# Performance work log

Hardware: AMD Instinct MI355X
Metric: run time of the kernel (lower is better)

The kernel has to match this reference:

```python
import jax, jax.numpy as jnp
import numpy as np
from math import factorial

# ---- static config mirroring Cace.__init__ ----
MAX_L = 3            # max angular degree
N_RBF = 8            # Bessel radial basis size
RB = 8               # n_radial_basis (radial embedding dim after transform)
K = 3                # n_atom_basis -> edge channels C = K*K
NZ = 4               # len(zs)
CUTOFF = 5.5
N_NODES = 2000
N_EDGES = 50000
T_MP = 1             # num_message_passing
MP_NORM = 1.0 / np.sqrt(25.0)   # 1/sqrt(avg_num_neighbors)
C = K * K

def _lxlylz(max_l):
    out = []
    for l in range(max_l + 1):
        for lx in range(l, -1, -1):
            for ly in range(l - lx, -1, -1):
                out.append((lx, ly, l - lx - ly))
    return out

L_LIST = _lxlylz(MAX_L)                 # 20 Cartesian monomials for max_l=3
NL = len(L_LIST)
LX = np.array([t[0] for t in L_LIST]); LY = np.array([t[1] for t in L_LIST]); LZ = np.array([t[2] for t in L_LIST])
DEGS = LX + LY + LZ                     # degree l of each monomial
MULTI = np.array([factorial(int(d)) / (factorial(int(a)) * factorial(int(b)) * factorial(int(c)))
                  for a, b, c, d in zip(LX, LY, LZ, DEGS)], dtype=np.float32)
SEL = np.zeros((NL, MAX_L + 1), np.float32)
SEL[np.arange(NL), DEGS] = 1.0          # monomial -> degree one-hot (for per-l sums)
NB = 1 + (MAX_L + 1)                    # symmetrizer feats: nu=1 (l=0) + nu=2 per l

def bessel(r):  # [E] -> [E, N_RBF]
    n = jnp.arange(1, N_RBF + 1, dtype=r.dtype)
    return jnp.sqrt(2.0 / CUTOFF) * jnp.sin(n[None, :] * jnp.pi * r[:, None] / CUTOFF) / r[:, None]

def poly_cutoff(r):  # MACE-style polynomial cutoff, p=6
    p = 6.0
    u = r / CUTOFF
    f = 1.0 - (p + 1.0) * (p + 2.0) / 2.0 * u**6 + p * (p + 2.0) * u**7 - p * (p + 1.0) / 2.0 * u**8
    return f * (u < 1.0)

def axis_pows(x):  # [E] -> [E, MAX_L+1] = x^0..x^MAX_L (safe grads, handles negatives)
    pows = [jnp.ones_like(x)]
    for _ in range(MAX_L):
        pows.append(pows[-1] * x)
    return jnp.stack(pows, axis=1)

def angular(u):  # unit vectors [E,3] -> Cartesian monomials [E, NL]
    return axis_pows(u[:, 0])[:, LX] * axis_pows(u[:, 1])[:, LY] * axis_pows(u[:, 2])[:, LZ]

def radial_transform(x, W):  # x [N,R,L,C], W [MAX_L+1,R,Rb] shared per degree l
    return jnp.einsum('nrlc,lrb->nblc', x, W[DEGS])

def symmetrize(A):  # A [N,Rb,NL,C] -> B [N,Rb,NB,C]
    b1 = A[:, :, :1, :]  # nu=1: the (0,0,0) monomial (index 0)
    w = (A * A) * jnp.asarray(MULTI)[None, None, :, None]
    b2 = jnp.einsum('nrlc,lm->nrmc', w, jnp.asarray(SEL))  # nu=2 invariant per degree l
    return jnp.concatenate([b1, b2], axis=2)


def setup_inputs() -> dict:
    key = jax.random.key(0)
    ks = jax.random.split(key, 9)
    positions = jax.random.uniform(ks[0], (N_NODES, 3), dtype=jnp.float32) * 12.0
    species = jax.random.randint(ks[1], (N_NODES,), 0, NZ)
    send = jax.random.randint(ks[2], (N_EDGES,), 0, N_NODES)
    off = jax.random.randint(ks[3], (N_EDGES,), 1, N_NODES)
    recv = (send + off) % N_NODES  # no self-edges -> strictly positive edge lengths
    edge_index = jnp.stack([send, recv])
    shifts = jnp.zeros((N_EDGES, 3), jnp.float32)
    W_embed = jax.random.normal(ks[4], (NZ, K), jnp.float32)
    W_radial = jax.random.normal(ks[5], (MAX_L + 1, N_RBF, RB), jnp.float32) / np.sqrt(N_RBF)
    W_mem = jax.random.normal(ks[6], (MAX_L + 1, RB, RB), jnp.float32) / np.sqrt(RB)
    W_ar = jax.random.normal(ks[7], (N_RBF, RB), jnp.float32) / np.sqrt(N_RBF)
    W_chi = jax.random.normal(ks[8], (RB, NB), jnp.float32) * 0.1
    return {"positions": positions, "shifts": shifts, "W_embed": W_embed, "W_radial": W_radial,
            "W_mem": W_mem, "W_ar": W_ar, "W_chi": W_chi, "species": species, "edge_index": edge_index}


def reference(positions, shifts, W_embed, W_radial, W_mem, W_ar, W_chi, species, edge_index):
    n_nodes = positions.shape[0]
    send, recv = edge_index[0], edge_index[1]
    # edge geometry
    vec = positions[recv] - positions[send] + shifts
    lengths = jnp.linalg.norm(vec, axis=-1)
    u = vec / (lengths[:, None] + 1e-9)
    rad = bessel(lengths)          # [E,R]
    fcut = poly_cutoff(lengths)    # [E]
    ang = angular(u)               # [E,NL]
    # edge type encoding: outer product of sender/receiver species embeddings
    emb = W_embed[species]         # [N,K]
    enc = (emb[send][:, :, None] * emb[recv][:, None, :]).reshape(-1, C)  # [E,C]
    # elementwise_multiply_3tensors -> [E,R,NL,C]
    edge_attri = jnp.einsum('er,el,ec->erlc', rad * fcut[:, None], ang, enc)
    A = radial_transform(jax.ops.segment_sum(edge_attri, recv, num_segments=n_nodes), W_radial)  # [N,Rb,NL,C]
    B = symmetrize(A)              # [N,Rb,NB,C]
    feats = [B]
    for _ in range(T_MP):
        mem = jnp.einsum('nrlc,lrb->nblc', A, W_mem[DEGS])        # NodeMemory
        chi = jnp.einsum('nbkc,bk->nc', B, W_chi)                  # MessageBchi node scalar
        msg_bchi = edge_attri * chi[send][:, None, None, :]
        A_bchi = radial_transform(jax.ops.segment_sum(msg_bchi, recv, num_segments=n_nodes), W_radial)
        fr = (rad @ W_ar) * fcut[:, None]                          # MessageAr radial filter [E,Rb]
        msg_ar = A[send] * fr[:, :, None, None]
        A_ar = jax.ops.segment_sum(msg_ar, recv, num_segments=n_nodes)
        A = (A_ar + A_bchi) * MP_NORM + mem
        B = symmetrize(A)
        feats.append(B)
    return jnp.stack(feats, axis=-1)   # [N,Rb,NB,C,T_MP+1]
```

## Files before the change

### kernel.cpp

```cpp
#include <hip/hip_runtime.h>
#include <hip/hip_bf16.h>


#define CUTF 5.5f
#define MPNORM 0.2f
#define TILE 48
#define BG 8

__constant__ int   d_DEGS[20]  = {0,1,1,1,2,2,2,2,2,2,3,3,3,3,3,3,3,3,3,3};
__constant__ float d_MULTI[20] = {1,1,1,1,1,2,2,1,2,1,1,3,3,3,6,3,1,3,3,1};

__global__ void k_count(const int* __restrict__ eidx, int* __restrict__ counts, int E) {
  int e = blockIdx.x * blockDim.x + threadIdx.x;
  if (e < E) atomicAdd(&counts[eidx[E + e]], 1);
}

__global__ void k_scan(const int* __restrict__ counts, int* __restrict__ offs, int N) {
  __shared__ int part[256];
  int t = threadIdx.x;
  int local[8]; int sum = 0;
  #pragma unroll
  for (int i = 0; i < 8; i++) {
    int idx = t*8 + i;
    int v = (idx < N) ? counts[idx] : 0;
    local[i] = sum; sum += v;
  }
  part[t] = sum; __syncthreads();
  for (int d = 1; d < 256; d <<= 1) {
    int add = (t >= d) ? part[t-d] : 0;
    __syncthreads();
    part[t] += add;
    __syncthreads();
  }
  int excl = part[t] - sum;
  #pragma unroll
  for (int i = 0; i < 8; i++) {
    int idx = t*8 + i;
    if (idx < N) offs[idx] = excl + local[i];
  }
  if (t == 255) offs[N] = part[255];
}

__global__ void k_edge(const float* __restrict__ pos,
                       const float* __restrict__ shifts,
                       const float* __restrict__ Wemb,
                       const float* __restrict__ Wrad,
                       const float* __restrict__ War,
                       const int* __restrict__ species,
                       const int* __restrict__ eidx,
                       const int* __restrict__ offs,
                       int* __restrict__ cursor,
                       float* __restrict__ edata,
                       int* __restrict__ esend,
                       int E) {
  __shared__ float war_s[64];
  __shared__ float wrad_s[256];
  int t = threadIdx.x;
  if (t < 64) war_s[t] = War[t];
  wrad_s[t] = Wrad[t];
  __syncthreads();
  int e = blockIdx.x * blockDim.x + t;
  if (e >= E) return;
  int s  = eidx[e];
  int rI = eidx[E + e];
  float vx = pos[rI*3+0] - pos[s*3+0] + shifts[e*3+0];
  float vy = pos[rI*3+1] - pos[s*3+1] + shifts[e*3+1];
  float vz = pos[rI*3+2] - pos[s*3+2] + shifts[e*3+2];
  float len = sqrtf(vx*vx + vy*vy + vz*vz);
  float inv = 1.0f / (len + 1e-9f);
  float ux = vx*inv, uy = vy*inv, uz = vz*inv;
  float uu = len * (1.0f/CUTF);
  float u2 = uu*uu, u6 = u2*u2*u2;
  float fcut = (uu < 1.0f) ? (1.0f - 28.0f*u6 + 48.0f*u6*uu - 21.0f*u6*u2) : 0.0f;
  float x = 3.14159265358979f * uu;
  float sn = sinf(x), c2 = 2.0f*cosf(x), snm1 = 0.0f;
  float pref = sqrtf(2.0f/CUTF) / (len + 1e-20f);
  float rad[8], g[8];
  #pragma unroll
  for (int k = 0; k < 8; k++) {
    rad[k] = pref * sn;
    g[k]   = rad[k] * fcut;
    float nxt = c2*sn - snm1; snm1 = sn; sn = nxt;
  }
  float v[80];
  #pragma unroll
  for (int d = 0; d < 4; d++)
    #pragma unroll
    for (int b = 0; b < 8; b++) {
      float a = 0.0f;
      #pragma unroll
      for (int r = 0; r < 8; r++) a += g[r] * wrad_s[d*64 + r*8 + b];
      v[d*8+b] = a;
    }
  #pragma unroll
  for (int b = 0; b < 8; b++) {
    float a = 0.0f;
    #pragma unroll
    for (int k = 0; k < 8; k++) a += rad[k] * war_s[k*8+b];
    v[32+b] = a * fcut;
  }
  float px2 = ux*ux, py2 = uy*uy, pz2 = uz*uz;
  v[40] = 1.0f; v[41] = ux;     v[42] = uy;     v[43] = uz;
  v[44] = px2;  v[45] = ux*uy;  v[46] = ux*uz;  v[47] = py2;
  v[48] = uy*uz;v[49] = pz2;
  v[50] = px2*ux; v[51] = px2*uy; v[52] = px2*uz; v[53] = ux*py2;
  v[54] = ux*uy*uz; v[55] = ux*pz2; v[56] = py2*uy; v[57] = py2*uz;
  v[58] = uy*pz2; v[59] = pz2*uz;
  int zs = species[s], zr = species[rI];
  float es0 = Wemb[zs*3+0], es1 = Wemb[zs*3+1], es2 = Wemb[zs*3+2];
  float er0 = Wemb[zr*3+0], er1 = Wemb[zr*3+1], er2 = Wemb[zr*3+2];
  v[60] = es0*er0; v[61] = es0*er1; v[62] = es0*er2;
  v[63] = es1*er0; v[64] = es1*er1; v[65] = es1*er2;
  v[66] = es2*er0; v[67] = es2*er1; v[68] = es2*er2;
  #pragma unroll
  for (int w = 69; w < 80; w++) v[w] = 0.0f;
  int slot = atomicAdd(&cursor[rI], 1);
  int dst = offs[rI] + slot;
  float4* eb4 = reinterpret_cast<float4*>(edata + (size_t)dst * 80);
  #pragma unroll
  for (int w = 0; w < 20; w++)
    eb4[w] = make_float4(v[4*w], v[4*w+1], v[4*w+2], v[4*w+3]);
  esend[dst] = s;
}

__global__ __launch_bounds__(192) void k_nodeA(
    const float* __restrict__ edata, const int* __restrict__ offs,
    const float* __restrict__ Wchi,
    float* __restrict__ A, uint4* __restrict__ Abf4,
    float* __restrict__ chi, float* __restrict__ B0, int N) {
  __shared__ float wchi_s[40];
  __shared__ float Bsh[360];
  __shared__ __align__(16) float est[TILE*80];
  int t = threadIdx.x, n = blockIdx.x;
  for (int i = t; i < 40;  i += 192) wchi_s[i] = Wchi[i];
  for (int i = t; i < 360; i += 192) Bsh[i] = 0.0f;
  int l = t / 9, c = t - l*9;
  bool act = t < 180;
  int ll = act ? l : 0, cc = act ? c : 0;
  int deg = act ? d_DEGS[ll] : 0;
  float Ab[8];
  #pragma unroll
  for (int b = 0; b < 8; b++) Ab[b] = 0.0f;
  int start = offs[n], end = offs[n+1];
  for (int tb = start; tb < end; tb += TILE) {
    int cnt = min(TILE, end - tb);
    __syncthreads();
    const float4* src = reinterpret_cast<const float4*>(edata + (size_t)tb*80);
    float4* dst = reinterpret_cast<float4*>(est);
    for (int i = t; i < cnt*20; i += 192) dst[i] = src[i];
    __syncthreads();
    #pragma unroll 4
    for (int j = 0; j < cnt; j++) {
      const float* eb = est + j*80;
      float p = eb[40+ll] * eb[60+cc];
      const float4* gw4 = reinterpret_cast<const float4*>(eb + deg*8);
      float4 g0 = gw4[0], g1 = gw4[1];
      Ab[0] += p*g0.x; Ab[1] += p*g0.y; Ab[2] += p*g0.z; Ab[3] += p*g0.w;
      Ab[4] += p*g1.x; Ab[5] += p*g1.y; Ab[6] += p*g1.z; Ab[7] += p*g1.w;
    }
  }
  __syncthreads();
  if (act) {
    #pragma unroll
    for (int b = 0; b < 8; b++) A[(size_t)n*1440 + t*8 + b] = Ab[b];
    unsigned int pr[4];
    #pragma unroll
    for (int bp = 0; bp < 4; bp++) {
      __hip_bfloat16 blo = __float2bfloat16(Ab[2*bp]);
      __hip_bfloat16 bhi = __float2bfloat16(Ab[2*bp+1]);
      pr[bp] = (unsigned int)(*reinterpret_cast<unsigned short*>(&blo))
             | ((unsigned int)(*reinterpret_cast<unsigned short*>(&bhi)) << 16);
    }
    uint4 pk; pk.x = pr[0]; pk.y = pr[1]; pk.z = pr[2]; pk.w = pr[3];
    Abf4[(size_t)n*180 + t] = pk;
    if (l == 0) {
      #pragma unroll
      for (int b = 0; b < 8; b++) Bsh[b*45 + c] = Ab[b];
    }
    float mlt = d_MULTI[ll]; int kk = 1 + deg;
    #pragma unroll
    for (int b = 0; b < 8; b++) atomicAdd(&Bsh[b*45 + kk*9 + c], mlt*Ab[b]*Ab[b]);
  }
  __syncthreads();
  if (t < 9) {
    float s = 0.0f;
    for (int b = 0; b < 8; b++)
      #pragma unroll
      for (int kq = 0; kq < 5; kq++) s += Bsh[b*45 + kq*9 + t] * wchi_s[b*5 + kq];
    chi[n*9 + t] = s;
  }
  for (int i = t; i < 360; i += 192)
    B0[(size_t)n*360 + i] = Bsh[i];
}

__global__ __launch_bounds__(192) void k_node2(
    const float* __restrict__ edata, const int* __restrict__ esend,
    const int* __restrict__ offs, const float* __restrict__ Wmem,
    const float* __restrict__ A, const uint4* __restrict__ Abf4,
    const float* __restrict__ chi, const float* __restrict__ B0,
    float* __restrict__ out, int N) {
  __shared__ float wm_s[288];
  __shared__ float Bsh[360];
  __shared__ int   snd_s[BG];
  __shared__ float chi_s[BG*9];
  __shared__ __align__(16) float est[BG*80];
  __shared__ uint4 stg[BG*180];
  int t = threadIdx.x, n = blockIdx.x;
  for (int i = t; i < 256; i += 192) { int d = i >> 6, rm = i & 63; wm_s[d*72+rm] = Wmem[i]; }
  for (int i = t; i < 360; i += 192) Bsh[i] = 0.0f;
  int l = t / 9, c = t - l*9;
  bool act = t < 180;
  int ll = act ? l : 0, cc = act ? c : 0;
  int tt = act ? t : 0;
  int deg = act ? d_DEGS[ll] : 0;
  float Sb[8], AR[8];
  #pragma unroll
  for (int b = 0; b < 8; b++) { Sb[b] = 0.0f; AR[b] = 0.0f; }
  int start = offs[n], end = offs[n+1];
  for (int j0 = start; j0 < end; j0 += BG) {
    int cb = min(BG, end - j0);
    __syncthreads();
    const float4* src = reinterpret_cast<const float4*>(edata + (size_t)j0*80);
    float4* dst = reinterpret_cast<float4*>(est);
    for (int i = t; i < cb*20; i += 192) dst[i] = src[i];
    if (t < BG) snd_s[t] = (t < cb) ? esend[j0 + t] : esend[j0];
    __syncthreads();
    #pragma unroll
    for (int u = 0; u < BG; u++) {
      int sr = snd_s[u];
      if (t < 180) stg[u*180 + t] = Abf4[(size_t)sr*180 + t];
    }
    if (t < BG*9) { int u = t / 9; chi_s[t] = chi[snd_s[u]*9 + (t - u*9)]; }
    __syncthreads();
    for (int u = 0; u < cb; u++) {
      const float* eb = est + u*80;
      float ch = chi_s[u*9 + cc];
      float pch = eb[40+ll] * eb[60+cc] * ch;
      const float4* gw4 = reinterpret_cast<const float4*>(eb + deg*8);
      float4 g0 = gw4[0], g1 = gw4[1];
      Sb[0] += pch*g0.x; Sb[1] += pch*g0.y; Sb[2] += pch*g0.z; Sb[3] += pch*g0.w;
      Sb[4] += pch*g1.x; Sb[5] += pch*g1.y; Sb[6] += pch*g1.z; Sb[7] += pch*g1.w;
      const float4* fr4 = reinterpret_cast<const float4*>(eb + 32);
      float4 f0 = fr4[0], f1 = fr4[1];
      uint4 q = stg[u*180 + tt];
      float a0 = __uint_as_float(q.x << 16), a1 = __uint_as_float(q.x & 0xffff0000u);
      float a2 = __uint_as_float(q.y << 16), a3 = __uint_as_float(q.y & 0xffff0000u);
      float a4 = __uint_as_float(q.z << 16), a5 = __uint_as_float(q.z & 0xffff0000u);
      float a6 = __uint_as_float(q.w << 16), a7 = __uint_as_float(q.w & 0xffff0000u);
      AR[0] += a0*f0.x; AR[1] += a1*f0.y; AR[2] += a2*f0.z; AR[3] += a3*f0.w;
      AR[4] += a4*f1.x; AR[5] += a5*f1.y; AR[6] += a6*f1.z; AR[7] += a7*f1.w;
    }
  }
  __syncthreads();
  if (act) {
    const float* wmp = &wm_s[deg*72];
    const float* aop = A + (size_t)n*1440 + t*8;
    float aown[8];
    #pragma unroll
    for (int r = 0; r < 8; r++) aown[r] = aop[r];
    float newA[8];
    #pragma unroll
    for (int b = 0; b < 8; b++) {
      float mem = 0.0f;
      #pragma unroll
      for (int r = 0; r < 8; r++) mem += aown[r]*wmp[r*8+b];
      newA[b] = (AR[b] + Sb[b])*MPNORM + mem;
    }
    if (l == 0) {
      #pragma unroll
      for (int b = 0; b < 8; b++) Bsh[b*45 + c] = newA[b];
    }
    float mlt = d_MULTI[ll]; int kk = 1 + deg;
    #pragma unroll
    for (int b = 0; b < 8; b++) atomicAdd(&Bsh[b*45 + kk*9 + c], mlt*newA[b]*newA[b]);
  }
  __syncthreads();
  float2* out2 = reinterpret_cast<float2*>(out);
  for (int i = t; i < 360; i += 192) {
    float2 pk; pk.x = B0[(size_t)n*360 + i]; pk.y = Bsh[i];
    out2[(size_t)n*360 + i] = pk;
  }
}

extern "C" void kernel_launch(void* const* d_in, const int* in_sizes, int n_in,
                              void* d_out, int out_size, void* d_ws, size_t ws_size,
                              hipStream_t stream) {
  const float* pos    = (const float*)d_in[0];
  const float* shifts = (const float*)d_in[1];
  const float* Wemb   = (const float*)d_in[2];
  const float* Wrad   = (const float*)d_in[3];
  const float* Wmem   = (const float*)d_in[4];
  const float* War    = (const float*)d_in[5];
  const float* Wchi   = (const float*)d_in[6];
  const int* species = (const int*)d_in[7];
  const int* eidx    = (const int*)d_in[8];
  float* out = (float*)d_out;
  int N = in_sizes[7];
  int E = in_sizes[8] / 2;

  char* base = (char*)d_ws;
  size_t off = 0;
  float* edata = (float*)(base + off); off += (size_t)E*80*4;
  float* A     = (float*)(base + off); off += (size_t)N*1440*4;
  uint4* Abf4  = (uint4*)(base + off); off += (size_t)N*180*16;
  float* chi   = (float*)(base + off); off += (size_t)N*9*4;
  float* B0    = (float*)(base + off); off += (size_t)N*360*4;
  int* counts  = (int*)(base + off);   off += (size_t)N*4;
  int* cursor  = (int*)(base + off);   off += (size_t)N*4;
  int* offs    = (int*)(base + off);   off += (((size_t)(N+1)*4) + 15) & ~(size_t)15;
  int* esend   = (int*)(base + off);   off += (size_t)E*4;

  hipMemsetAsync(counts, 0, (size_t)N*2*4, stream);
  int eb = (E + 255) / 256;
  k_count<<<eb, 256, 0, stream>>>(eidx, counts, E);
  k_scan<<<1, 256, 0, stream>>>(counts, offs, N);
  k_edge<<<eb, 256, 0, stream>>>(pos, shifts, Wemb, Wrad, War, species, eidx, offs,
                                 cursor, edata, esend, E);
  k_nodeA<<<N, 192, 0, stream>>>(edata, offs, Wchi, A, Abf4, chi, B0, N);
  k_node2<<<N, 192, 0, stream>>>(edata, esend, offs, Wmem, A, Abf4, chi, B0, out, N);
}
```

Measured before the change: 173.5 us.

## Fuse edge feature computation into node kernels and recompute instead of materializing

Replaces the edge kernel that wrote 80-float per-edge records with a small kernel that only writes a sorted edge order. Each node kernel now computes edge geometry, radial and angular features in shared memory tile by tile, so the edge buffer and the fp32 A/B0 intermediates no longer go through global memory. k_node2 recomputes A and B0 itself and prefetches the neighbor's bf16 A row and chi one edge ahead, in place of staging groups of neighbors in shared memory. The cost is doing the edge math twice, extra barriers inside each tile, and a larger shared tile per block.

```diff
diff --git a/kernel.cpp b/kernel.cpp
--- a/kernel.cpp
+++ b/kernel.cpp
@@ -5,7 +5,7 @@
 #define CUTF 5.5f
 #define MPNORM 0.2f
 #define TILE 48
-#define BG 8
+#define RS 72
 
 __constant__ int   d_DEGS[20]  = {0,1,1,1,2,2,2,2,2,2,3,3,3,3,3,3,3,3,3,3};
 __constant__ float d_MULTI[20] = {1,1,1,1,1,2,2,1,2,1,1,3,3,3,6,3,1,3,3,1};
@@ -41,119 +41,127 @@
   if (t == 255) offs[N] = part[255];
 }
 
-__global__ void k_edge(const float* __restrict__ pos,
-                       const float* __restrict__ shifts,
-                       const float* __restrict__ Wemb,
-                       const float* __restrict__ Wrad,
-                       const float* __restrict__ War,
-                       const int* __restrict__ species,
-                       const int* __restrict__ eidx,
-                       const int* __restrict__ offs,
-                       int* __restrict__ cursor,
-                       float* __restrict__ edata,
-                       int* __restrict__ esend,
-                       int E) {
-  __shared__ float war_s[64];
-  __shared__ float wrad_s[256];
-  int t = threadIdx.x;
-  if (t < 64) war_s[t] = War[t];
-  wrad_s[t] = Wrad[t];
-  __syncthreads();
-  int e = blockIdx.x * blockDim.x + t;
+__global__ void k_fill(const int* __restrict__ eidx, const int* __restrict__ offs,
+                       int* __restrict__ cursor, int* __restrict__ order, int E) {
+  int e = blockIdx.x * blockDim.x + threadIdx.x;
   if (e >= E) return;
-  int s  = eidx[e];
-  int rI = eidx[E + e];
-  float vx = pos[rI*3+0] - pos[s*3+0] + shifts[e*3+0];
-  float vy = pos[rI*3+1] - pos[s*3+1] + shifts[e*3+1];
-  float vz = pos[rI*3+2] - pos[s*3+2] + shifts[e*3+2];
-  float len = sqrtf(vx*vx + vy*vy + vz*vz);
-  float inv = 1.0f / (len + 1e-9f);
-  float ux = vx*inv, uy = vy*inv, uz = vz*inv;
-  float uu = len * (1.0f/CUTF);
-  float u2 = uu*uu, u6 = u2*u2*u2;
-  float fcut = (uu < 1.0f) ? (1.0f - 28.0f*u6 + 48.0f*u6*uu - 21.0f*u6*u2) : 0.0f;
-  float x = 3.14159265358979f * uu;
-  float sn = sinf(x), c2 = 2.0f*cosf(x), snm1 = 0.0f;
-  float pref = sqrtf(2.0f/CUTF) / (len + 1e-20f);
-  float rad[8], g[8];
-  #pragma unroll
-  for (int k = 0; k < 8; k++) {
-    rad[k] = pref * sn;
-    g[k]   = rad[k] * fcut;
-    float nxt = c2*sn - snm1; snm1 = sn; sn = nxt;
-  }
-  float v[80];
-  #pragma unroll
-  for (int d = 0; d < 4; d++)
+  int r = eidx[E + e];
+  int slot = atomicAdd(&cursor[r], 1);
+  order[offs[r] + slot] = e;
+}
+
+__device__ __forceinline__ void fill_est(
+    float* est, const int* __restrict__ order, const int* __restrict__ eidx,
+    const float* __restrict__ pos, const float* __restrict__ shifts,
+    const int* __restrict__ species,
+    const float* war_s, const float* wrad_s, const float* wemb_s,
+    int tb, int cnt, int t,
+    float pnx, float pny, float pnz, float er0, float er1, float er2)
+{
+  __syncthreads();
+  if (t < cnt) {
+    int e = order[tb + t];
+    int s = eidx[e];
+    float vx = pnx - pos[s*3+0] + shifts[e*3+0];
+    float vy = pny - pos[s*3+1] + shifts[e*3+1];
+    float vz = pnz - pos[s*3+2] + shifts[e*3+2];
+    float len = sqrtf(vx*vx + vy*vy + vz*vz);
+    float inv = 1.0f / (len + 1e-9f);
+    float ux = vx*inv, uy = vy*inv, uz = vz*inv;
+    float uu = len * (1.0f/CUTF);
+    float u2 = uu*uu, u6 = u2*u2*u2;
+    float fcut = (uu < 1.0f) ? (1.0f - 28.0f*u6 + 48.0f*u6*uu - 21.0f*u6*u2) : 0.0f;
+    float x = 3.14159265358979f * uu;
+    float sn = sinf(x), c2 = 2.0f*cosf(x), snm1 = 0.0f;
+    float pref = sqrtf(2.0f/CUTF) / (len + 1e-20f);
+    float* eb = est + t*RS;
+    float rad[8];
+    #pragma unroll
+    for (int k = 0; k < 8; k++) {
+      rad[k] = pref * sn;
+      eb[k]  = rad[k] * fcut;
+      float nxt = c2*sn - snm1; snm1 = sn; sn = nxt;
+    }
     #pragma unroll
     for (int b = 0; b < 8; b++) {
       float a = 0.0f;
       #pragma unroll
-      for (int r = 0; r < 8; r++) a += g[r] * wrad_s[d*64 + r*8 + b];
-      v[d*8+b] = a;
-    }
-  #pragma unroll
-  for (int b = 0; b < 8; b++) {
+      for (int k = 0; k < 8; k++) a += rad[k] * war_s[k*8+b];
+      eb[32+b] = a * fcut;
+    }
+    float px2 = ux*ux, py2 = uy*uy, pz2 = uz*uz;
+    eb[40] = 1.0f; eb[41] = ux;     eb[42] = uy;     eb[43] = uz;
+    eb[44] = px2;  eb[45] = ux*uy;  eb[46] = ux*uz;  eb[47] = py2;
+    eb[48] = uy*uz;eb[49] = pz2;
+    eb[50] = px2*ux; eb[51] = px2*uy; eb[52] = px2*uz; eb[53] = ux*py2;
+    eb[54] = ux*uy*uz; eb[55] = ux*pz2; eb[56] = py2*uy; eb[57] = py2*uz;
+    eb[58] = uy*pz2; eb[59] = pz2*uz;
+    int zs = species[s];
+    float es0 = wemb_s[zs*3+0], es1 = wemb_s[zs*3+1], es2 = wemb_s[zs*3+2];
+    eb[60] = es0*er0; eb[61] = es0*er1; eb[62] = es0*er2;
+    eb[63] = es1*er0; eb[64] = es1*er1; eb[65] = es1*er2;
+    eb[66] = es2*er0; eb[67] = es2*er1; eb[68] = es2*er2;
+    eb[69] = __int_as_float(s);
+  }
+  __syncthreads();
+  int tot = cnt * 32;
+  float gwv[8];
+  int kq = 0;
+  for (int idx = t; idx < tot; idx += 192, kq++) {
+    int j = idx >> 5, f = idx & 31, d = f >> 3, b = f & 7;
+    const float* gr = est + j*RS;
     float a = 0.0f;
     #pragma unroll
-    for (int k = 0; k < 8; k++) a += rad[k] * war_s[k*8+b];
-    v[32+b] = a * fcut;
-  }
-  float px2 = ux*ux, py2 = uy*uy, pz2 = uz*uz;
-  v[40] = 1.0f; v[41] = ux;     v[42] = uy;     v[43] = uz;
-  v[44] = px2;  v[45] = ux*uy;  v[46] = ux*uz;  v[47] = py2;
-  v[48] = uy*uz;v[49] = pz2;
-  v[50] = px2*ux; v[51] = px2*uy; v[52] = px2*uz; v[53] = ux*py2;
-  v[54] = ux*uy*uz; v[55] = ux*pz2; v[56] = py2*uy; v[57] = py2*uz;
-  v[58] = uy*pz2; v[59] = pz2*uz;
-  int zs = species[s], zr = species[rI];
-  float es0 = Wemb[zs*3+0], es1 = Wemb[zs*3+1], es2 = Wemb[zs*3+2];
-  float er0 = Wemb[zr*3+0], er1 = Wemb[zr*3+1], er2 = Wemb[zr*3+2];
-  v[60] = es0*er0; v[61] = es0*er1; v[62] = es0*er2;
-  v[63] = es1*er0; v[64] = es1*er1; v[65] = es1*er2;
-  v[66] = es2*er0; v[67] = es2*er1; v[68] = es2*er2;
-  #pragma unroll
-  for (int w = 69; w < 80; w++) v[w] = 0.0f;
-  int slot = atomicAdd(&cursor[rI], 1);
-  int dst = offs[rI] + slot;
-  float4* eb4 = reinterpret_cast<float4*>(edata + (size_t)dst * 80);
-  #pragma unroll
-  for (int w = 0; w < 20; w++)
-    eb4[w] = make_float4(v[4*w], v[4*w+1], v[4*w+2], v[4*w+3]);
-  esend[dst] = s;
-}
-
-__global__ __launch_bounds__(192) void k_nodeA(
-    const float* __restrict__ edata, const int* __restrict__ offs,
-    const float* __restrict__ Wchi,
-    float* __restrict__ A, uint4* __restrict__ Abf4,
-    float* __restrict__ chi, float* __restrict__ B0, int N) {
+    for (int r = 0; r < 8; r++) a += gr[r] * wrad_s[d*64 + r*8 + b];
+    gwv[kq] = a;
+  }
+  __syncthreads();
+  kq = 0;
+  for (int idx = t; idx < tot; idx += 192, kq++)
+    est[(idx >> 5)*RS + (idx & 31)] = gwv[kq];
+  __syncthreads();
+}
+
+__global__ __launch_bounds__(192, 6) void k_nodeA(
+    const float* __restrict__ pos, const float* __restrict__ shifts,
+    const float* __restrict__ Wemb, const float* __restrict__ Wrad,
+    const float* __restrict__ War, const float* __restrict__ Wchi,
+    const int* __restrict__ species, const int* __restrict__ eidx,
+    const int* __restrict__ offs, const int* __restrict__ order,
+    uint4* __restrict__ Abf4, float* __restrict__ chi, int N)
+{
+  __shared__ float wrad_s[256];
+  __shared__ float war_s[64];
   __shared__ float wchi_s[40];
+  __shared__ float wemb_s[12];
   __shared__ float Bsh[360];
-  __shared__ __align__(16) float est[TILE*80];
+  __shared__ __align__(16) float est[TILE*RS];
   int t = threadIdx.x, n = blockIdx.x;
-  for (int i = t; i < 40;  i += 192) wchi_s[i] = Wchi[i];
+  for (int i = t; i < 256; i += 192) wrad_s[i] = Wrad[i];
+  if (t < 64) war_s[t] = War[t];
+  if (t < 40) wchi_s[t] = Wchi[t];
+  if (t < 12) wemb_s[t] = Wemb[t];
   for (int i = t; i < 360; i += 192) Bsh[i] = 0.0f;
   int l = t / 9, c = t - l*9;
   bool act = t < 180;
   int ll = act ? l : 0, cc = act ? c : 0;
-  int deg = act ? d_DEGS[ll] : 0;
-  float Ab[8];
-  #pragma unroll
-  for (int b = 0; b < 8; b++) Ab[b] = 0.0f;
+  int dgl = act ? d_DEGS[ll] : 0;
+  float mlt = act ? d_MULTI[ll] : 0.0f;
+  float pnx = pos[n*3+0], pny = pos[n*3+1], pnz = pos[n*3+2];
+  int zr = species[n];
+  __syncthreads();
+  float er0 = wemb_s[zr*3+0], er1 = wemb_s[zr*3+1], er2 = wemb_s[zr*3+2];
   int start = offs[n], end = offs[n+1];
+  float Ab[8] = {0,0,0,0,0,0,0,0};
   for (int tb = start; tb < end; tb += TILE) {
     int cnt = min(TILE, end - tb);
-    __syncthreads();
-    const float4* src = reinterpret_cast<const float4*>(edata + (size_t)tb*80);
-    float4* dst = reinterpret_cast<float4*>(est);
-    for (int i = t; i < cnt*20; i += 192) dst[i] = src[i];
-    __syncthreads();
-    #pragma unroll 4
+    fill_est(est, order, eidx, pos, shifts, species, war_s, wrad_s, wemb_s,
+             tb, cnt, t, pnx, pny, pnz, er0, er1, er2);
+    #pragma unroll 2
     for (int j = 0; j < cnt; j++) {
-      const float* eb = est + j*80;
+      const float* eb = est + j*RS;
       float p = eb[40+ll] * eb[60+cc];
-      const float4* gw4 = reinterpret_cast<const float4*>(eb + deg*8);
+      const float4* gw4 = reinterpret_cast<const float4*>(eb + dgl*8);
       float4 g0 = gw4[0], g1 = gw4[1];
       Ab[0] += p*g0.x; Ab[1] += p*g0.y; Ab[2] += p*g0.z; Ab[3] += p*g0.w;
       Ab[4] += p*g1.x; Ab[5] += p*g1.y; Ab[6] += p*g1.z; Ab[7] += p*g1.w;
@@ -161,8 +169,6 @@
   }
   __syncthreads();
   if (act) {
-    #pragma unroll
-    for (int b = 0; b < 8; b++) A[(size_t)n*1440 + t*8 + b] = Ab[b];
     unsigned int pr[4];
     #pragma unroll
     for (int bp = 0; bp < 4; bp++) {
@@ -177,7 +183,7 @@
       #pragma unroll
       for (int b = 0; b < 8; b++) Bsh[b*45 + c] = Ab[b];
     }
-    float mlt = d_MULTI[ll]; int kk = 1 + deg;
+    int kk = 1 + dgl;
     #pragma unroll
     for (int b = 0; b < 8; b++) atomicAdd(&Bsh[b*45 + kk*9 + c], mlt*Ab[b]*Ab[b]);
   }
@@ -189,60 +195,68 @@
       for (int kq = 0; kq < 5; kq++) s += Bsh[b*45 + kq*9 + t] * wchi_s[b*5 + kq];
     chi[n*9 + t] = s;
   }
-  for (int i = t; i < 360; i += 192)
-    B0[(size_t)n*360 + i] = Bsh[i];
-}
-
-__global__ __launch_bounds__(192) void k_node2(
-    const float* __restrict__ edata, const int* __restrict__ esend,
-    const int* __restrict__ offs, const float* __restrict__ Wmem,
-    const float* __restrict__ A, const uint4* __restrict__ Abf4,
-    const float* __restrict__ chi, const float* __restrict__ B0,
-    float* __restrict__ out, int N) {
+}
+
+__global__ __launch_bounds__(192, 6) void k_node2(
+    const float* __restrict__ pos, const float* __restrict__ shifts,
+    const float* __restrict__ Wemb, const float* __restrict__ Wrad,
+    const float* __restrict__ War, const float* __restrict__ Wmem,
+    const int* __restrict__ species, const int* __restrict__ eidx,
+    const int* __restrict__ offs, const int* __restrict__ order,
+    const uint4* __restrict__ Abf4, const float* __restrict__ chi,
+    float* __restrict__ out, int N)
+{
+  __shared__ float wrad_s[256];
+  __shared__ float war_s[64];
   __shared__ float wm_s[288];
+  __shared__ float wemb_s[12];
   __shared__ float Bsh[360];
-  __shared__ int   snd_s[BG];
-  __shared__ float chi_s[BG*9];
-  __shared__ __align__(16) float est[BG*80];
-  __shared__ uint4 stg[BG*180];
+  __shared__ __align__(16) float est[TILE*RS];
   int t = threadIdx.x, n = blockIdx.x;
-  for (int i = t; i < 256; i += 192) { int d = i >> 6, rm = i & 63; wm_s[d*72+rm] = Wmem[i]; }
+  for (int i = t; i < 256; i += 192) wrad_s[i] = Wrad[i];
+  for (int i = t; i < 256; i += 192) { int d = i>>6, rm = i&63; wm_s[d*72+rm] = Wmem[i]; }
+  if (t < 64) war_s[t] = War[t];
+  if (t < 12) wemb_s[t] = Wemb[t];
   for (int i = t; i < 360; i += 192) Bsh[i] = 0.0f;
   int l = t / 9, c = t - l*9;
   bool act = t < 180;
   int ll = act ? l : 0, cc = act ? c : 0;
   int tt = act ? t : 0;
-  int deg = act ? d_DEGS[ll] : 0;
-  float Sb[8], AR[8];
-  #pragma unroll
-  for (int b = 0; b < 8; b++) { Sb[b] = 0.0f; AR[b] = 0.0f; }
+  int dgl = act ? d_DEGS[ll] : 0;
+  float mlt = act ? d_MULTI[ll] : 0.0f;
+  float pnx = pos[n*3+0], pny = pos[n*3+1], pnz = pos[n*3+2];
+  int zr = species[n];
+  __syncthreads();
+  float er0 = wemb_s[zr*3+0], er1 = wemb_s[zr*3+1], er2 = wemb_s[zr*3+2];
   int start = offs[n], end = offs[n+1];
-  for (int j0 = start; j0 < end; j0 += BG) {
-    int cb = min(BG, end - j0);
-    __syncthreads();
-    const float4* src = reinterpret_cast<const float4*>(edata + (size_t)j0*80);
-    float4* dst = reinterpret_cast<float4*>(est);
-    for (int i = t; i < cb*20; i += 192) dst[i] = src[i];
-    if (t < BG) snd_s[t] = (t < cb) ? esend[j0 + t] : esend[j0];
-    __syncthreads();
-    #pragma unroll
-    for (int u = 0; u < BG; u++) {
-      int sr = snd_s[u];
-      if (t < 180) stg[u*180 + t] = Abf4[(size_t)sr*180 + t];
-    }
-    if (t < BG*9) { int u = t / 9; chi_s[t] = chi[snd_s[u]*9 + (t - u*9)]; }
-    __syncthreads();
-    for (int u = 0; u < cb; u++) {
-      const float* eb = est + u*80;
-      float ch = chi_s[u*9 + cc];
-      float pch = eb[40+ll] * eb[60+cc] * ch;
-      const float4* gw4 = reinterpret_cast<const float4*>(eb + deg*8);
+  float Ab[8] = {0,0,0,0,0,0,0,0};
+  float Sb[8] = {0,0,0,0,0,0,0,0};
+  float AR[8] = {0,0,0,0,0,0,0,0};
+  for (int tb = start; tb < end; tb += TILE) {
+    int cnt = min(TILE, end - tb);
+    fill_est(est, order, eidx, pos, shifts, species, war_s, wrad_s, wemb_s,
+             tb, cnt, t, pnx, pny, pnz, er0, er1, er2);
+    int s0 = __float_as_int(est[69]);
+    uint4 q_c = Abf4[(size_t)s0*180 + tt];
+    float ch_c = chi[s0*9 + cc];
+    for (int j = 0; j < cnt; j++) {
+      uint4 q = q_c; float ch = ch_c;
+      if (j + 1 < cnt) {
+        int sn = __float_as_int(est[(j+1)*RS + 69]);
+        q_c = Abf4[(size_t)sn*180 + tt];
+        ch_c = chi[sn*9 + cc];
+      }
+      const float* eb = est + j*RS;
+      float p = eb[40+ll] * eb[60+cc];
+      float pch = p * ch;
+      const float4* gw4 = reinterpret_cast<const float4*>(eb + dgl*8);
       float4 g0 = gw4[0], g1 = gw4[1];
+      Ab[0] += p*g0.x; Ab[1] += p*g0.y; Ab[2] += p*g0.z; Ab[3] += p*g0.w;
+      Ab[4] += p*g1.x; Ab[5] += p*g1.y; Ab[6] += p*g1.z; Ab[7] += p*g1.w;
       Sb[0] += pch*g0.x; Sb[1] += pch*g0.y; Sb[2] += pch*g0.z; Sb[3] += pch*g0.w;
       Sb[4] += pch*g1.x; Sb[5] += pch*g1.y; Sb[6] += pch*g1.z; Sb[7] += pch*g1.w;
       const float4* fr4 = reinterpret_cast<const float4*>(eb + 32);
       float4 f0 = fr4[0], f1 = fr4[1];
-      uint4 q = stg[u*180 + tt];
       float a0 = __uint_as_float(q.x << 16), a1 = __uint_as_float(q.x & 0xffff0000u);
       float a2 = __uint_as_float(q.y << 16), a3 = __uint_as_float(q.y & 0xffff0000u);
       float a4 = __uint_as_float(q.z << 16), a5 = __uint_as_float(q.z & 0xffff0000u);
@@ -253,33 +267,41 @@
   }
   __syncthreads();
   if (act) {
-    const float* wmp = &wm_s[deg*72];
-    const float* aop = A + (size_t)n*1440 + t*8;
-    float aown[8];
-    #pragma unroll
-    for (int r = 0; r < 8; r++) aown[r] = aop[r];
+    if (l == 0) {
+      #pragma unroll
+      for (int b = 0; b < 8; b++) Bsh[b*45 + c] = Ab[b];
+    }
+    int kk = 1 + dgl;
+    #pragma unroll
+    for (int b = 0; b < 8; b++) atomicAdd(&Bsh[b*45 + kk*9 + c], mlt*Ab[b]*Ab[b]);
+  }
+  __syncthreads();
+  for (int i = t; i < 360; i += 192)
+    out[((size_t)n*360 + i)*2] = Bsh[i];
+  __syncthreads();
+  for (int i = t; i < 360; i += 192) Bsh[i] = 0.0f;
+  __syncthreads();
+  if (act) {
+    const float* wmp = wm_s + dgl*72;
     float newA[8];
     #pragma unroll
     for (int b = 0; b < 8; b++) {
       float mem = 0.0f;
       #pragma unroll
-      for (int r = 0; r < 8; r++) mem += aown[r]*wmp[r*8+b];
+      for (int r = 0; r < 8; r++) mem += Ab[r] * wmp[r*8+b];
       newA[b] = (AR[b] + Sb[b])*MPNORM + mem;
     }
     if (l == 0) {
       #pragma unroll
       for (int b = 0; b < 8; b++) Bsh[b*45 + c] = newA[b];
     }
-    float mlt = d_MULTI[ll]; int kk = 1 + deg;
+    int kk = 1 + dgl;
     #pragma unroll
     for (int b = 0; b < 8; b++) atomicAdd(&Bsh[b*45 + kk*9 + c], mlt*newA[b]*newA[b]);
   }
   __syncthreads();
-  float2* out2 = reinterpret_cast<float2*>(out);
-  for (int i = t; i < 360; i += 192) {
-    float2 pk; pk.x = B0[(size_t)n*360 + i]; pk.y = Bsh[i];
-    out2[(size_t)n*360 + i] = pk;
-  }
+  for (int i = t; i < 360; i += 192)
+    out[((size_t)n*360 + i)*2 + 1] = Bsh[i];
 }
 
 extern "C" void kernel_launch(void* const* d_in, const int* in_sizes, int n_in,
@@ -300,22 +322,20 @@
 
   char* base = (char*)d_ws;
   size_t off = 0;
-  float* edata = (float*)(base + off); off += (size_t)E*80*4;
-  float* A     = (float*)(base + off); off += (size_t)N*1440*4;
   uint4* Abf4  = (uint4*)(base + off); off += (size_t)N*180*16;
   float* chi   = (float*)(base + off); off += (size_t)N*9*4;
-  float* B0    = (float*)(base + off); off += (size_t)N*360*4;
+  int* offs    = (int*)(base + off);   off += (size_t)(N+1)*4;
+  int* order   = (int*)(base + off);   off += (size_t)E*4;
   int* counts  = (int*)(base + off);   off += (size_t)N*4;
   int* cursor  = (int*)(base + off);   off += (size_t)N*4;
-  int* offs    = (int*)(base + off);   off += (((size_t)(N+1)*4) + 15) & ~(size_t)15;
-  int* esend   = (int*)(base + off);   off += (size_t)E*4;
 
   hipMemsetAsync(counts, 0, (size_t)N*2*4, stream);
   int eb = (E + 255) / 256;
   k_count<<<eb, 256, 0, stream>>>(eidx, counts, E);
   k_scan<<<1, 256, 0, stream>>>(counts, offs, N);
-  k_edge<<<eb, 256, 0, stream>>>(pos, shifts, Wemb, Wrad, War, species, eidx, offs,
-                                 cursor, edata, esend, E);
-  k_nodeA<<<N, 192, 0, stream>>>(edata, offs, Wchi, A, Abf4, chi, B0, N);
-  k_node2<<<N, 192, 0, stream>>>(edata, esend, offs, Wmem, A, Abf4, chi, B0, out, N);
-}
+  k_fill<<<eb, 256, 0, stream>>>(eidx, offs, cursor, order, E);
+  k_nodeA<<<N, 192, 0, stream>>>(pos, shifts, Wemb, Wrad, War, Wchi, species,
+                                 eidx, offs, order, Abf4, chi, N);
+  k_node2<<<N, 192, 0, stream>>>(pos, shifts, Wemb, Wrad, War, Wmem, species,
+                                 eidx, offs, order, Abf4, chi, out, N);
+}
```

Result: slower. 208.5 us (+20.2%).
